# Optimization experiments

Hardware: AMD Instinct MI355X
Metric: run time of the kernel (lower is better)

Reference implementation:

```python
import jax, jax.numpy as jnp
import numpy as np

MARGIN = 0.3
EPS = 1e-12


def setup_inputs() -> dict:
    key = jax.random.key(0)
    k1, k2, k3 = jax.random.split(key, 3)
    B, D = 8192, 1024
    features = jax.random.normal(k1, (B, D), dtype=jnp.float32)
    labels = jax.random.randint(k2, (B,), 0, 100, dtype=jnp.int64)
    domain_labels = jax.random.randint(k3, (B,), 0, 2, dtype=jnp.int64)
    return {"features": features, "labels": labels, "domain_labels": domain_labels}


def reference(features, labels, domain_labels):
    # L2-normalize rows (F.normalize: x / max(||x||, eps))
    norm = jnp.maximum(jnp.linalg.norm(features, axis=1, keepdims=True), EPS)
    f = features / norm

    herb = domain_labels == 0   # [B] anchors
    field = domain_labels == 1  # [B] candidates

    sq = jnp.sum(f * f, axis=1)                                   # [B]
    d2 = sq[:, None] + sq[None, :] - 2.0 * jnp.einsum('id,jd->ij', f, f)
    d = jnp.sqrt(jnp.maximum(d2, 0.0))                            # [B, B]

    same = labels[:, None] == labels[None, :]                     # [B, B]
    pair = herb[:, None] & field[None, :]
    pos_mask = pair & same
    neg_mask = pair & ~same

    INF = jnp.float32(jnp.inf)
    pos_min = jnp.min(jnp.where(pos_mask, d, INF), axis=1)        # [B]
    neg_min = jnp.min(jnp.where(neg_mask, d, INF), axis=1)        # [B]

    valid = herb & jnp.any(pos_mask, axis=1) & jnp.any(neg_mask, axis=1)
    # Substitute 0 for invalid rows BEFORE subtracting to avoid inf - inf.
    pos_s = jnp.where(valid, pos_min, 0.0)
    neg_s = jnp.where(valid, neg_min, 0.0)
    tl = jnp.maximum(pos_s - neg_s + MARGIN, 0.0)                 # [B]

    loss_sum = jnp.sum(jnp.where(valid, tl, 0.0))
    count = jnp.sum(valid.astype(jnp.float32))
    return jnp.where(count > 0, loss_sum / jnp.maximum(count, 1.0), 0.0)
```

## Files before the change

### kernel.cpp

```cpp
#include <hip/hip_runtime.h>


#define B_ROWS 8192
#define DIM    1024

typedef __bf16 bf16x8 __attribute__((ext_vector_type(8)));
typedef float  f32x4  __attribute__((ext_vector_type(4)));

__device__ __forceinline__ unsigned short f2bf_rne(float x) {
    unsigned u = __float_as_uint(x);
    unsigned r = (u + 0x7FFFu + ((u >> 16) & 1u)) >> 16;
    return (unsigned short)r;
}
__device__ __forceinline__ float bf2f(unsigned short h) {
    return __uint_as_float(((unsigned)h) << 16);
}

__device__ __forceinline__ void async_copy16(const void* g, void* l) {
    __builtin_amdgcn_global_load_lds(
        (const __attribute__((address_space(1))) unsigned int*)g,
        (__attribute__((address_space(3))) unsigned int*)l,
        16, 0, 0);
}

__global__ __launch_bounds__(256) void compute_slots(
    const int* __restrict__ dom, int* __restrict__ slotOf,
    unsigned* __restrict__ cnt)
{
    __shared__ int cnts[256];
    __shared__ int base[257];
    const int t = threadIdx.x;
    const int p0 = t * 32;

    unsigned mask = 0u; int c = 0;
    #pragma unroll
    for (int i = 0; i < 32; ++i) {
        const int isA = (dom[p0 + i] == 0) ? 1 : 0;
        mask |= ((unsigned)isA) << i;
        c += isA;
    }
    cnts[t] = c;
    __syncthreads();
    if (t == 0) {
        int acc = 0;
        for (int i = 0; i < 256; ++i) { base[i] = acc; acc += cnts[i]; }
        base[256] = acc;
        cnt[0] = (unsigned)acc;
    }
    __syncthreads();
    const int nA = base[256];
    int aB = base[t];
    #pragma unroll
    for (int i = 0; i < 32; ++i) {
        const int isA = (mask >> i) & 1;
        slotOf[p0 + i] = isA ? aB : nA + (p0 + i - aB);
        aB += isA;
    }
}

__global__ __launch_bounds__(256) void normalize_rows(
    const float* __restrict__ feat, const int* __restrict__ labels,
    const int* __restrict__ slotOf, unsigned short* __restrict__ G,
    int* __restrict__ labG, float* __restrict__ sqG)
{
    const int wv = threadIdx.x >> 6, lane = threadIdx.x & 63;
    const int row = blockIdx.x * 4 + wv;

    const float4* src = (const float4*)(feat + (size_t)row * DIM);
    float4 v[4];
    float ss = 0.0f;
    #pragma unroll
    for (int j = 0; j < 4; ++j) {
        v[j] = src[j * 64 + lane];
        ss += v[j].x * v[j].x + v[j].y * v[j].y + v[j].z * v[j].z + v[j].w * v[j].w;
    }
    #pragma unroll
    for (int s = 32; s > 0; s >>= 1) ss += __shfl_xor(ss, s);
    const float inv = 1.0f / fmaxf(sqrtf(ss), 1e-12f);

    const int slot = slotOf[row];
    unsigned short ub[16];
    float ss2 = 0.0f;
    #pragma unroll
    for (int j = 0; j < 4; ++j) {
        const float f0 = v[j].x * inv, f1 = v[j].y * inv,
                    f2 = v[j].z * inv, f3 = v[j].w * inv;
        ub[j * 4 + 0] = f2bf_rne(f0); ub[j * 4 + 1] = f2bf_rne(f1);
        ub[j * 4 + 2] = f2bf_rne(f2); ub[j * 4 + 3] = f2bf_rne(f3);
        #pragma unroll
        for (int q = 0; q < 4; ++q) {
            const float fr = bf2f(ub[j * 4 + q]);
            ss2 += fr * fr;
        }
    }
    #pragma unroll
    for (int s = 32; s > 0; s >>= 1) ss2 += __shfl_xor(ss2, s);
    if (lane == 0) {
        sqG[slot]  = ss2;
        labG[slot] = labels[row];
    }
    ushort4* dst = (ushort4*)(G + (size_t)slot * DIM);
    #pragma unroll
    for (int j = 0; j < 4; ++j) {
        ushort4 pk;
        pk.x = ub[j * 4 + 0]; pk.y = ub[j * 4 + 1];
        pk.z = ub[j * 4 + 2]; pk.w = ub[j * 4 + 3];
        dst[j * 64 + lane] = pk;
    }
}

__global__ __launch_bounds__(256) void tile_mindist(
    const unsigned short* __restrict__ G, const int* __restrict__ labG,
    const float* __restrict__ sqG, const unsigned* __restrict__ cnt,
    unsigned* __restrict__ posmin, unsigned* __restrict__ negmin)
{
    const int nA = (int)cnt[0];
    const int nF = B_ROWS - nA;
    const int nTA = (nA + 127) >> 7;
    const int nTF = (nF + 127) >> 7;
    const int total = nTA * nTF;

    __shared__ __align__(16) unsigned short S[2][2][128 * 32];

    const int t = threadIdx.x;
    const int lane = t & 63, w = t >> 6;
    const int wm = w >> 1, wn = w & 1;
    const int l15 = lane & 15, quad = lane >> 4;

    const int ch0 = 2 * w;
    const int crow = lane >> 2;
    const int cbyte = (lane & 3) * 16;

    const int rdA = (wm * 64 + l15) * 32 + quad * 8;
    const int rdF = (wn * 64 + l15) * 32 + quad * 8;

    const char* Gb = (const char*)G;

    for (int tile = blockIdx.x; tile < total; tile += gridDim.x) {
        const int tx = tile % nTA;
        const int ty = tile / nTA;
        const int rowA0 = tx * 128;
        const int rowF0 = nA + ty * 128;

        const char* ga[2]; const char* gf[2];
        #pragma unroll
        for (int h = 0; h < 2; ++h) {
            const int ch = ch0 + h;
            const int rA = rowA0 + 16 * ch + crow;
            int rF = rowF0 + 16 * ch + crow;
            if (rF > B_ROWS - 1) rF = B_ROWS - 1;
            ga[h] = Gb + (size_t)rA * (DIM * 2) + cbyte;
            gf[h] = Gb + (size_t)rF * (DIM * 2) + cbyte;
        }

        f32x4 acc[4][4] = {};

        #pragma unroll
        for (int h = 0; h < 2; ++h) {
            async_copy16(ga[h], &S[0][0][(ch0 + h) * 512]);
            async_copy16(gf[h], &S[0][1][(ch0 + h) * 512]);
        }
        __syncthreads();

        #pragma unroll 4
        for (int step = 0; step < 32; ++step) {
            const int cur = step & 1;
            const int nb = cur ^ 1;
            if (step < 31) {
                const int off = (step + 1) * 64;
                #pragma unroll
                for (int h = 0; h < 2; ++h) {
                    async_copy16(ga[h] + off, &S[nb][0][(ch0 + h) * 512]);
                    async_copy16(gf[h] + off, &S[nb][1][(ch0 + h) * 512]);
                }
            }

            const unsigned short* pa = &S[cur][0][rdA];
            const unsigned short* pf = &S[cur][1][rdF];
            bf16x8 a[4], b[4];
            #pragma unroll
            for (int fm = 0; fm < 4; ++fm) a[fm] = *(const bf16x8*)(pa + fm * 512);
            #pragma unroll
            for (int fn = 0; fn < 4; ++fn) b[fn] = *(const bf16x8*)(pf + fn * 512);
            #pragma unroll
            for (int fm = 0; fm < 4; ++fm)
                #pragma unroll
                for (int fn = 0; fn < 4; ++fn)
                    acc[fm][fn] = __builtin_amdgcn_mfma_f32_16x16x32_bf16(
                        a[fm], b[fn], acc[fm][fn], 0, 0, 0);

            __syncthreads();
        }

        const float INFV = __uint_as_float(0x7f800000u);
        float sqf[4]; int lf_[4]; bool vf[4];
        #pragma unroll
        for (int fn = 0; fn < 4; ++fn) {
            const int rf = rowF0 + wn * 64 + fn * 16 + l15;
            vf[fn] = rf < B_ROWS;
            const int rc = vf[fn] ? rf : (B_ROWS - 1);
            sqf[fn] = sqG[rc];
            lf_[fn] = labG[rc];
        }
        #pragma unroll
        for (int fm = 0; fm < 4; ++fm) {
            #pragma unroll
            for (int r = 0; r < 4; ++r) {
                const int ra = rowA0 + wm * 64 + fm * 16 + quad * 4 + r;
                const bool va = ra < nA;
                const int rac = va ? ra : 0;
                const float sqa = sqG[rac];
                const int la_ = labG[rac];
                float pmin = INFV, nmin = INFV;
                #pragma unroll
                for (int fn = 0; fn < 4; ++fn) {
                    const float dd = fmaxf(sqa + sqf[fn] - 2.0f * acc[fm][fn][r], 0.0f);
                    if (vf[fn]) {
                        if (la_ == lf_[fn]) pmin = fminf(pmin, dd);
                        else                nmin = fminf(nmin, dd);
                    }
                }
                #pragma unroll
                for (int s = 1; s < 16; s <<= 1) {
                    pmin = fminf(pmin, __shfl_xor(pmin, s));
                    nmin = fminf(nmin, __shfl_xor(nmin, s));
                }
                if (l15 == 0 && va) {
                    if (pmin < INFV) atomicMin(&posmin[ra], __float_as_uint(pmin));
                    if (nmin < INFV) atomicMin(&negmin[ra], __float_as_uint(nmin));
                }
            }
        }
        __syncthreads();
    }
}

__global__ __launch_bounds__(256) void reduce_loss(
    const unsigned* __restrict__ posmin, const unsigned* __restrict__ negmin,
    float* __restrict__ accum)
{
    const int i = blockIdx.x * 256 + threadIdx.x;
    const unsigned up = posmin[i], un = negmin[i];
    float tl = 0.0f, c = 0.0f;
    if (up != 0xFFFFFFFFu && un != 0xFFFFFFFFu) {
        const float pd = sqrtf(__uint_as_float(up));
        const float nd = sqrtf(__uint_as_float(un));
        tl = fmaxf(pd - nd + 0.3f, 0.0f);
        c = 1.0f;
    }
    #pragma unroll
    for (int s = 32; s > 0; s >>= 1) {
        tl += __shfl_down(tl, s);
        c  += __shfl_down(c, s);
    }
    __shared__ float sb[8];
    const int lane = threadIdx.x & 63, w = threadIdx.x >> 6;
    if (lane == 0) { sb[w] = tl; sb[4 + w] = c; }
    __syncthreads();
    if (threadIdx.x == 0) {
        atomicAdd(&accum[0], sb[0] + sb[1] + sb[2] + sb[3]);
        atomicAdd(&accum[1], sb[4] + sb[5] + sb[6] + sb[7]);
    }
}

__global__ void finalize(const float* __restrict__ accum, float* __restrict__ out) {
    const float s = accum[0], c = accum[1];
    out[0] = (c > 0.0f) ? s / fmaxf(c, 1.0f) : 0.0f;
}

extern "C" void kernel_launch(void* const* d_in, const int* in_sizes, int n_in,
                              void* d_out, int out_size, void* d_ws, size_t ws_size,
                              hipStream_t stream) {
    const float* feat  = (const float*)d_in[0];
    const int* labels  = (const int*)d_in[1];
    const int* dom     = (const int*)d_in[2];
    float* out = (float*)d_out;

    char* ws = (char*)d_ws;
    unsigned short* G   = (unsigned short*)(ws);
    int*      labG      = (int*)(ws + 16777216);
    float*    sqG       = (float*)(ws + 16809984);
    unsigned* posmin    = (unsigned*)(ws + 16842752);
    unsigned* negmin    = (unsigned*)(ws + 16875520);
    unsigned* cnt       = (unsigned*)(ws + 16908288);
    float*    accum     = (float*)(ws + 16908296);
    int*      slotOf    = (int*)(ws + 16842752);

    hipMemsetAsync(cnt, 0, 16, stream);

    compute_slots<<<1, 256, 0, stream>>>(dom, slotOf, cnt);
    normalize_rows<<<B_ROWS / 4, 256, 0, stream>>>(feat, labels, slotOf,
                                                   G, labG, sqG);

    hipMemsetAsync(posmin, 0xFF, 65536, stream);

    tile_mindist<<<1056, 256, 0, stream>>>(G, labG, sqG, cnt, posmin, negmin);

    reduce_loss<<<B_ROWS / 256, 256, 0, stream>>>(posmin, negmin, accum);
    finalize<<<1, 1, 0, stream>>>(accum, out);
}
```

Before: 179.1 us.

## Enlarge GEMM tiles to 256x256 with 4-stage LDS pipeline and swizzled layout

```diff
diff --git a/kernel.cpp b/kernel.cpp
--- a/kernel.cpp
+++ b/kernel.cpp
@@ -30,31 +30,43 @@
     __shared__ int cnts[256];
     __shared__ int base[257];
     const int t = threadIdx.x;
-    const int p0 = t * 32;
 
     unsigned mask = 0u; int c = 0;
     #pragma unroll
     for (int i = 0; i < 32; ++i) {
-        const int isA = (dom[p0 + i] == 0) ? 1 : 0;
+        const int isA = (dom[t + 256 * i] == 0) ? 1 : 0;
         mask |= ((unsigned)isA) << i;
         c += isA;
     }
     cnts[t] = c;
     __syncthreads();
-    if (t == 0) {
-        int acc = 0;
-        for (int i = 0; i < 256; ++i) { base[i] = acc; acc += cnts[i]; }
-        base[256] = acc;
-        cnt[0] = (unsigned)acc;
+    if (t < 64) {
+        const int c0 = cnts[4 * t + 0], c1 = cnts[4 * t + 1];
+        const int c2 = cnts[4 * t + 2], c3 = cnts[4 * t + 3];
+        const int s4 = c0 + c1 + c2 + c3;
+        int sc = s4;
+        #pragma unroll
+        for (int d = 1; d < 64; d <<= 1) {
+            const int o = __shfl_up(sc, d);
+            if (t >= d) sc += o;
+        }
+        const int b = sc - s4;
+        base[4 * t + 0] = b;
+        base[4 * t + 1] = b + c0;
+        base[4 * t + 2] = b + c0 + c1;
+        base[4 * t + 3] = b + c0 + c1 + c2;
+        if (t == 63) { base[256] = sc; cnt[0] = (unsigned)sc; }
     }
     __syncthreads();
     const int nA = base[256];
     int aB = base[t];
+    int fB = nA + t * 32 - base[t];
     #pragma unroll
     for (int i = 0; i < 32; ++i) {
         const int isA = (mask >> i) & 1;
-        slotOf[p0 + i] = isA ? aB : nA + (p0 + i - aB);
+        slotOf[t + 256 * i] = isA ? aB : fB;
         aB += isA;
+        fB += 1 - isA;
     }
 }
 
@@ -109,87 +121,110 @@
     }
 }
 
-__global__ __launch_bounds__(256) void tile_mindist(
+__global__ __launch_bounds__(512, 2) void tile_mindist(
     const unsigned short* __restrict__ G, const int* __restrict__ labG,
     const float* __restrict__ sqG, const unsigned* __restrict__ cnt,
     unsigned* __restrict__ posmin, unsigned* __restrict__ negmin)
 {
     const int nA = (int)cnt[0];
     const int nF = B_ROWS - nA;
-    const int nTA = (nA + 127) >> 7;
-    const int nTF = (nF + 127) >> 7;
+    const int nTA = (nA + 255) >> 8;
+    const int nTF = (nF + 255) >> 8;
     const int total = nTA * nTF;
 
-    __shared__ __align__(16) unsigned short S[2][2][128 * 32];
+    __shared__ __align__(16) unsigned short S[4][2][256 * 32];
 
     const int t = threadIdx.x;
     const int lane = t & 63, w = t >> 6;
-    const int wm = w >> 1, wn = w & 1;
+    const int wm = w >> 2, wn = w & 3;
     const int l15 = lane & 15, quad = lane >> 4;
-
-    const int ch0 = 2 * w;
-    const int crow = lane >> 2;
-    const int cbyte = (lane & 3) * 16;
-
-    const int rdA = (wm * 64 + l15) * 32 + quad * 8;
-    const int rdF = (wn * 64 + l15) * 32 + quad * 8;
+    const int ch8 = (quad ^ (l15 & 3)) * 8;
+
+    const int srow  = lane >> 2;
+    const int scs16 = (((lane & 3) ^ (srow & 3)) << 4);
 
     const char* Gb = (const char*)G;
+    const int rAq = wm * 128 + l15;
+    const int rFq = wn * 64  + l15;
 
     for (int tile = blockIdx.x; tile < total; tile += gridDim.x) {
         const int tx = tile % nTA;
         const int ty = tile / nTA;
-        const int rowA0 = tx * 128;
-        const int rowF0 = nA + ty * 128;
-
-        const char* ga[2]; const char* gf[2];
-        #pragma unroll
-        for (int h = 0; h < 2; ++h) {
-            const int ch = ch0 + h;
-            const int rA = rowA0 + 16 * ch + crow;
-            int rF = rowF0 + 16 * ch + crow;
-            if (rF > B_ROWS - 1) rF = B_ROWS - 1;
-            ga[h] = Gb + (size_t)rA * (DIM * 2) + cbyte;
-            gf[h] = Gb + (size_t)rF * (DIM * 2) + cbyte;
-        }
-
-        f32x4 acc[4][4] = {};
-
-        #pragma unroll
-        for (int h = 0; h < 2; ++h) {
-            async_copy16(ga[h], &S[0][0][(ch0 + h) * 512]);
-            async_copy16(gf[h], &S[0][1][(ch0 + h) * 512]);
-        }
-        __syncthreads();
-
-        #pragma unroll 4
-        for (int step = 0; step < 32; ++step) {
-            const int cur = step & 1;
-            const int nb = cur ^ 1;
-            if (step < 31) {
-                const int off = (step + 1) * 64;
+        const int rowA0 = tx << 8;
+        const int rowF0 = nA + (ty << 8);
+
+        const int arow = rowA0 + 32 * w + srow;
+        const int frow = rowF0 + 32 * w + srow;
+
+        f32x4 acc[8][4] = {};
+
+        #pragma unroll
+        for (int p = 0; p < 2; ++p) {
+            const int ktB = p * 64;
+            #pragma unroll
+            for (int h = 0; h < 2; ++h) {
+                const char* gA = Gb + (size_t)(arow + 16 * h) * 2048 + ktB + scs16;
+                async_copy16(gA, &S[p][0][(32 * w + 16 * h) * 32]);
+                int rF = frow + 16 * h; if (rF > B_ROWS - 1) rF = B_ROWS - 1;
+                const char* gF = Gb + (size_t)rF * 2048 + ktB + scs16;
+                async_copy16(gF, &S[p][1][(32 * w + 16 * h) * 32]);
+            }
+        }
+        asm volatile("s_waitcnt vmcnt(4)" ::: "memory");
+        __builtin_amdgcn_s_barrier();
+        __builtin_amdgcn_sched_barrier(0);
+
+        for (int kt = 0; kt < 32; ++kt) {
+            const unsigned short* SA = &S[kt & 3][0][0];
+            const unsigned short* SF = &S[kt & 3][1][0];
+
+            bf16x8 a[8], f[4];
+            #pragma unroll
+            for (int fm = 0; fm < 4; ++fm)
+                a[fm] = *(const bf16x8*)(SA + (rAq + fm * 16) * 32 + ch8);
+            #pragma unroll
+            for (int fn = 0; fn < 4; ++fn)
+                f[fn] = *(const bf16x8*)(SF + (rFq + fn * 16) * 32 + ch8);
+            if (kt < 30) {
+                unsigned short* DA = &S[(kt + 2) & 3][0][0];
+                unsigned short* DF = &S[(kt + 2) & 3][1][0];
+                const int ktB = (kt + 2) * 64;
                 #pragma unroll
                 for (int h = 0; h < 2; ++h) {
-                    async_copy16(ga[h] + off, &S[nb][0][(ch0 + h) * 512]);
-                    async_copy16(gf[h] + off, &S[nb][1][(ch0 + h) * 512]);
+                    const char* gA = Gb + (size_t)(arow + 16 * h) * 2048 + ktB + scs16;
+                    async_copy16(gA, DA + (32 * w + 16 * h) * 32);
+                    int rF = frow + 16 * h; if (rF > B_ROWS - 1) rF = B_ROWS - 1;
+                    const char* gF = Gb + (size_t)rF * 2048 + ktB + scs16;
+                    async_copy16(gF, DF + (32 * w + 16 * h) * 32);
                 }
             }
-
-            const unsigned short* pa = &S[cur][0][rdA];
-            const unsigned short* pf = &S[cur][1][rdF];
-            bf16x8 a[4], b[4];
-            #pragma unroll
-            for (int fm = 0; fm < 4; ++fm) a[fm] = *(const bf16x8*)(pa + fm * 512);
-            #pragma unroll
-            for (int fn = 0; fn < 4; ++fn) b[fn] = *(const bf16x8*)(pf + fn * 512);
+            __builtin_amdgcn_s_barrier();
+            __builtin_amdgcn_s_setprio(1);
             #pragma unroll
             for (int fm = 0; fm < 4; ++fm)
                 #pragma unroll
                 for (int fn = 0; fn < 4; ++fn)
                     acc[fm][fn] = __builtin_amdgcn_mfma_f32_16x16x32_bf16(
-                        a[fm], b[fn], acc[fm][fn], 0, 0, 0);
-
-            __syncthreads();
+                        a[fm], f[fn], acc[fm][fn], 0, 0, 0);
+            __builtin_amdgcn_s_setprio(0);
+            __builtin_amdgcn_s_barrier();
+
+            #pragma unroll
+            for (int fm = 4; fm < 8; ++fm)
+                a[fm] = *(const bf16x8*)(SA + (rAq + fm * 16) * 32 + ch8);
+            if (kt < 30) { asm volatile("s_waitcnt vmcnt(4)" ::: "memory"); }
+            else         { asm volatile("s_waitcnt vmcnt(0)" ::: "memory"); }
+            __builtin_amdgcn_s_barrier();
+            __builtin_amdgcn_s_setprio(1);
+            #pragma unroll
+            for (int fm = 4; fm < 8; ++fm)
+                #pragma unroll
+                for (int fn = 0; fn < 4; ++fn)
+                    acc[fm][fn] = __builtin_amdgcn_mfma_f32_16x16x32_bf16(
+                        a[fm], f[fn], acc[fm][fn], 0, 0, 0);
+            __builtin_amdgcn_s_setprio(0);
+            __builtin_amdgcn_s_barrier();
+            __builtin_amdgcn_sched_barrier(0);
         }
 
         const float INFV = __uint_as_float(0x7f800000u);
@@ -203,10 +238,10 @@
             lf_[fn] = labG[rc];
         }
         #pragma unroll
-        for (int fm = 0; fm < 4; ++fm) {
+        for (int fm = 0; fm < 8; ++fm) {
             #pragma unroll
             for (int r = 0; r < 4; ++r) {
-                const int ra = rowA0 + wm * 64 + fm * 16 + quad * 4 + r;
+                const int ra = rowA0 + wm * 128 + fm * 16 + quad * 4 + r;
                 const bool va = ra < nA;
                 const int rac = va ? ra : 0;
                 const float sqa = sqG[rac];
@@ -231,7 +266,6 @@
                 }
             }
         }
-        __syncthreads();
     }
 }
 
@@ -294,7 +328,7 @@
 
     hipMemsetAsync(posmin, 0xFF, 65536, stream);
 
-    tile_mindist<<<1056, 256, 0, stream>>>(G, labG, sqG, cnt, posmin, negmin);
+    tile_mindist<<<272, 512, 0, stream>>>(G, labG, sqG, cnt, posmin, negmin);
 
     reduce_loss<<<B_ROWS / 256, 256, 0, stream>>>(posmin, negmin, accum);
     finalize<<<1, 1, 0, stream>>>(accum, out);
```

Result: slower. 193.8 us (+8.2%).

## Deepen GEMM LDS pipeline to four buffers with two-step prefetch and partial waits

Applied to the files above, without the earlier changes.

```diff
diff --git a/kernel.cpp b/kernel.cpp
--- a/kernel.cpp
+++ b/kernel.cpp
@@ -30,31 +30,43 @@
     __shared__ int cnts[256];
     __shared__ int base[257];
     const int t = threadIdx.x;
-    const int p0 = t * 32;
 
     unsigned mask = 0u; int c = 0;
     #pragma unroll
     for (int i = 0; i < 32; ++i) {
-        const int isA = (dom[p0 + i] == 0) ? 1 : 0;
+        const int isA = (dom[t + 256 * i] == 0) ? 1 : 0;
         mask |= ((unsigned)isA) << i;
         c += isA;
     }
     cnts[t] = c;
     __syncthreads();
-    if (t == 0) {
-        int acc = 0;
-        for (int i = 0; i < 256; ++i) { base[i] = acc; acc += cnts[i]; }
-        base[256] = acc;
-        cnt[0] = (unsigned)acc;
+    if (t < 64) {
+        const int c0 = cnts[4 * t + 0], c1 = cnts[4 * t + 1];
+        const int c2 = cnts[4 * t + 2], c3 = cnts[4 * t + 3];
+        const int s4 = c0 + c1 + c2 + c3;
+        int sc = s4;
+        #pragma unroll
+        for (int d = 1; d < 64; d <<= 1) {
+            const int o = __shfl_up(sc, d);
+            if (t >= d) sc += o;
+        }
+        const int b = sc - s4;
+        base[4 * t + 0] = b;
+        base[4 * t + 1] = b + c0;
+        base[4 * t + 2] = b + c0 + c1;
+        base[4 * t + 3] = b + c0 + c1 + c2;
+        if (t == 63) { base[256] = sc; cnt[0] = (unsigned)sc; }
     }
     __syncthreads();
     const int nA = base[256];
     int aB = base[t];
+    int fB = nA + t * 32 - base[t];
     #pragma unroll
     for (int i = 0; i < 32; ++i) {
         const int isA = (mask >> i) & 1;
-        slotOf[p0 + i] = isA ? aB : nA + (p0 + i - aB);
+        slotOf[t + 256 * i] = isA ? aB : fB;
         aB += isA;
+        fB += 1 - isA;
     }
 }
 
@@ -120,7 +132,7 @@
     const int nTF = (nF + 127) >> 7;
     const int total = nTA * nTF;
 
-    __shared__ __align__(16) unsigned short S[2][2][128 * 32];
+    __shared__ __align__(16) unsigned short S[4][2][128 * 32];
 
     const int t = threadIdx.x;
     const int lane = t & 63, w = t >> 6;
@@ -156,18 +168,21 @@
         f32x4 acc[4][4] = {};
 
         #pragma unroll
-        for (int h = 0; h < 2; ++h) {
-            async_copy16(ga[h], &S[0][0][(ch0 + h) * 512]);
-            async_copy16(gf[h], &S[0][1][(ch0 + h) * 512]);
-        }
-        __syncthreads();
+        for (int p = 0; p < 2; ++p) {
+            #pragma unroll
+            for (int h = 0; h < 2; ++h) {
+                async_copy16(ga[h] + p * 64, &S[p][0][(ch0 + h) * 512]);
+                async_copy16(gf[h] + p * 64, &S[p][1][(ch0 + h) * 512]);
+            }
+        }
+        asm volatile("s_waitcnt vmcnt(4)" ::: "memory");
+        __builtin_amdgcn_s_barrier();
 
         #pragma unroll 4
         for (int step = 0; step < 32; ++step) {
-            const int cur = step & 1;
-            const int nb = cur ^ 1;
-            if (step < 31) {
-                const int off = (step + 1) * 64;
+            if (step < 30) {
+                const int nb = (step + 2) & 3;
+                const int off = (step + 2) * 64;
                 #pragma unroll
                 for (int h = 0; h < 2; ++h) {
                     async_copy16(ga[h] + off, &S[nb][0][(ch0 + h) * 512]);
@@ -175,8 +190,9 @@
                 }
             }
 
-            const unsigned short* pa = &S[cur][0][rdA];
-            const unsigned short* pf = &S[cur][1][rdF];
+            const int cb = step & 3;
+            const unsigned short* pa = &S[cb][0][rdA];
+            const unsigned short* pf = &S[cb][1][rdF];
             bf16x8 a[4], b[4];
             #pragma unroll
             for (int fm = 0; fm < 4; ++fm) a[fm] = *(const bf16x8*)(pa + fm * 512);
@@ -189,7 +205,9 @@
                     acc[fm][fn] = __builtin_amdgcn_mfma_f32_16x16x32_bf16(
                         a[fm], b[fn], acc[fm][fn], 0, 0, 0);
 
-            __syncthreads();
+            if (step < 30) { asm volatile("s_waitcnt vmcnt(4)" ::: "memory"); }
+            else           { asm volatile("s_waitcnt vmcnt(0)" ::: "memory"); }
+            __builtin_amdgcn_s_barrier();
         }
 
         const float INFV = __uint_as_float(0x7f800000u);
@@ -231,7 +249,6 @@
                 }
             }
         }
-        __syncthreads();
     }
 }
 
```

Result: slower. 210.1 us (+17.3%).
